# Optimization experiments

Measured on AMD Instinct MI355X. Metric: run time of the kernel, lower is better.

## Reference

```python
import jax, jax.numpy as jnp
import numpy as np

BN_EPS = 1e-5


def setup_inputs() -> dict:
    key = jax.random.key(0)
    ks = jax.random.split(key, 6)
    b, c_out, c_high = 8, 256, 512
    h1 = w1 = 64
    h2 = w2 = 32
    return {
        "fms_low": jax.random.normal(ks[0], (b, c_out, h1, w1), jnp.float32),
        "fms_high": jax.random.normal(ks[1], (b, c_high, h2, w2), jnp.float32),
        "w_conv": jax.random.normal(ks[2], (c_out, c_high), jnp.float32) * (1.0 / np.sqrt(c_high)),
        "bn_gamma": jnp.ones((c_out,), jnp.float32),
        "bn_beta": jnp.zeros((c_out,), jnp.float32),
        "bn_mean": jnp.zeros((c_out,), jnp.float32),
        "bn_var": jnp.ones((c_out,), jnp.float32),
        "fc1_w": jax.random.normal(ks[3], (c_out // 4, c_out), jnp.float32) * (1.0 / np.sqrt(c_out)),
        "fc1_b": jnp.zeros((c_out // 4,), jnp.float32),
        "fc2_w": jax.random.normal(ks[4], (c_out // 4, c_out), jnp.float32) * (1.0 / np.sqrt(c_out)),
        "fc2_b": jnp.zeros((c_out // 4,), jnp.float32),
        "scale": jax.random.normal(ks[5], (1,), jnp.float32),
    }


def reference(fms_low, fms_high, w_conv, bn_gamma, bn_beta, bn_mean, bn_var,
              fc1_w, fc1_b, fc2_w, fc2_b, scale):
    b, c, h1, w1 = fms_low.shape
    # conv_high: 1x1 conv (no bias) + BN (inference) + ReLU
    x = jnp.einsum('bchw,oc->bohw', fms_high, w_conv)  # [b, 256, h2, w2]
    inv = bn_gamma / jnp.sqrt(bn_var + BN_EPS)
    x = x * inv[None, :, None, None] + (bn_beta - bn_mean * inv)[None, :, None, None]
    x = jax.nn.relu(x)
    # raw row-major reshapes, matching torch .view(b, -1, C)
    feat_low = fms_low.reshape(b, -1, c)    # [b, N_low, 256]
    feat_high = x.reshape(b, -1, c)         # [b, N_high, 256]
    mid_low = feat_low @ fc1_w.T + fc1_b    # [b, N_low, 64]
    mid_high = feat_high @ fc2_w.T + fc2_b  # [b, N_high, 64]
    energy = jnp.einsum('bnd,bmd->bnm', mid_low, mid_high)  # [b, N_low, N_high]
    attn = jax.nn.softmax(energy, axis=-1)
    # bmm(feat_high^T, attn^T) -> [b, 256, N_low]
    mid = jnp.einsum('bmc,bnm->bcn', feat_high, attn).reshape(b, c, h1, w1)
    return scale[0] * mid
```

## Files before the change

kernel.cpp:

```cpp
#include <hip/hip_runtime.h>
#include <hip/hip_bf16.h>

typedef __bf16 v8bf __attribute__((ext_vector_type(8)));
typedef float  v4f  __attribute__((ext_vector_type(4)));

typedef __attribute__((address_space(3))) void       lds_vd;
typedef __attribute__((address_space(1))) const void gbl_vd;

#define MFMA16(a, b, c) __builtin_amdgcn_mfma_f32_16x16x32_bf16(a, b, c, 0, 0, 0)

__device__ __forceinline__ void split_hl(float v, __bf16* h, __bf16* l) {
    __bf16 hh = (__bf16)v;
    *h = hh;
    *l = (__bf16)(v - (float)hh);
}

__device__ __forceinline__ int swz_idx(int row, int col) {
    return row * 64 + ((((col >> 3) ^ (row & 7))) << 3) + (col & 7);
}
__device__ __forceinline__ const __bf16* frag_ptr(const __bf16* base, int row, int g) {
    return base + row * 64 + ((g ^ (row & 7)) << 3);
}


__global__ __launch_bounds__(256) void k_conv(
    const float* __restrict__ FH, const float* __restrict__ W,
    const float* __restrict__ gamma, const float* __restrict__ beta,
    const float* __restrict__ mean, const float* __restrict__ var,
    __bf16* __restrict__ Xhi, __bf16* __restrict__ Xlo, __bf16* __restrict__ VT)
{
    __shared__ __align__(16) __bf16 Ah[64 * 64];
    __shared__ __align__(16) __bf16 Al[64 * 64];
    __shared__ __align__(16) __bf16 Bh[64 * 64];
    __shared__ __align__(16) __bf16 Bl[64 * 64];
    __shared__ float invl[64], shl[64];

    const int tid = threadIdx.x, lane = tid & 63, w = tid >> 6;
    const int l15 = lane & 15, quad = lane >> 4;
    const int u0 = blockIdx.x * 16, o0 = blockIdx.y * 64, b = blockIdx.z;
    const float* FHb = FH + (size_t)b * 524288;

    if (tid < 64) {
        const int o = o0 + tid;
        const float iv = gamma[o] * rsqrtf(var[o] + 1e-5f);
        invl[tid] = iv;
        shl[tid] = beta[o] - mean[o] * iv;
    }

    const int ao = tid >> 2, aseg = tid & 3;
    float wreg[16], freg[16];
    {
        const float* wp = W + (size_t)(o0 + ao) * 512 + aseg * 16;
        #pragma unroll
        for (int q = 0; q < 4; ++q) {
            float4 f = ((const float4*)wp)[q];
            wreg[4*q] = f.x; wreg[4*q+1] = f.y; wreg[4*q+2] = f.z; wreg[4*q+3] = f.w;
        }
        const float* fp = FHb + (size_t)lane * 1024 + w * 256 + u0;
        #pragma unroll
        for (int q = 0; q < 4; ++q) {
            float4 f = ((const float4*)fp)[q];
            freg[4*q] = f.x; freg[4*q+1] = f.y; freg[4*q+2] = f.z; freg[4*q+3] = f.w;
        }
    }

    v4f acc[2][2];
    #pragma unroll
    for (int i = 0; i < 2; ++i)
        #pragma unroll
        for (int j = 0; j < 2; ++j) { v4f z = {0.f,0.f,0.f,0.f}; acc[i][j] = z; }
    const int oh = w >> 1, nh = w & 1;

    for (int ch = 0; ch < 8; ++ch) {
        if (ch) __syncthreads();
        #pragma unroll
        for (int z = 0; z < 2; ++z) {
            v8bf hv, lv;
            #pragma unroll
            for (int e = 0; e < 8; ++e) {
                __bf16 h, l; split_hl(wreg[8*z + e], &h, &l);
                hv[e] = h; lv[e] = l;
            }
            const int gi = (2*aseg + z) ^ (ao & 7);
            *(v8bf*)(Ah + ao*64 + (gi << 3)) = hv;
            *(v8bf*)(Al + ao*64 + (gi << 3)) = lv;
        }
        #pragma unroll
        for (int ul = 0; ul < 16; ++ul) {
            __bf16 h, l; split_hl(freg[ul], &h, &l);
            const int idx = (w*16 + ul)*64 + (((lane >> 3) ^ (ul & 7)) << 3) + (lane & 7);
            Bh[idx] = h; Bl[idx] = l;
        }
        __syncthreads();
        if (ch < 7) {
            const int c1 = (ch + 1) * 64;
            const float* wp = W + (size_t)(o0 + ao) * 512 + c1 + aseg * 16;
            #pragma unroll
            for (int q = 0; q < 4; ++q) {
                float4 f = ((const float4*)wp)[q];
                wreg[4*q] = f.x; wreg[4*q+1] = f.y; wreg[4*q+2] = f.z; wreg[4*q+3] = f.w;
            }
            const float* fp = FHb + (size_t)(c1 + lane) * 1024 + w * 256 + u0;
            #pragma unroll
            for (int q = 0; q < 4; ++q) {
                float4 f = ((const float4*)fp)[q];
                freg[4*q] = f.x; freg[4*q+1] = f.y; freg[4*q+2] = f.z; freg[4*q+3] = f.w;
            }
        }
        #pragma unroll
        for (int ks = 0; ks < 2; ++ks) {
            const int g = 4*ks + quad;
            v8bf a_h[2], a_l[2], b_h[2], b_l[2];
            #pragma unroll
            for (int i = 0; i < 2; ++i) {
                const int row = oh*32 + i*16 + l15;
                a_h[i] = *(const v8bf*)frag_ptr(Ah, row, g);
                a_l[i] = *(const v8bf*)frag_ptr(Al, row, g);
            }
            #pragma unroll
            for (int j = 0; j < 2; ++j) {
                const int row = nh*32 + j*16 + l15;
                b_h[j] = *(const v8bf*)frag_ptr(Bh, row, g);
                b_l[j] = *(const v8bf*)frag_ptr(Bl, row, g);
            }
            #pragma unroll
            for (int i = 0; i < 2; ++i)
                #pragma unroll
                for (int j = 0; j < 2; ++j) {
                    acc[i][j] = MFMA16(a_h[i], b_h[j], acc[i][j]);
                    acc[i][j] = MFMA16(a_h[i], b_l[j], acc[i][j]);
                    acc[i][j] = MFMA16(a_l[i], b_h[j], acc[i][j]);
                }
        }
    }
    __syncthreads();

    #pragma unroll
    for (int i = 0; i < 2; ++i)
        #pragma unroll
        for (int j = 0; j < 2; ++j)
            #pragma unroll
            for (int r = 0; r < 4; ++r) {
                const int row = oh*32 + i*16 + quad*4 + r;
                const int col = nh*32 + j*16 + l15;
                float v = acc[i][j][r] * invl[row] + shl[row];
                v = fmaxf(v, 0.f);
                __bf16 h, l; split_hl(v, &h, &l);
                const int idx = swz_idx(row, col);
                Ah[idx] = h; Al[idx] = l;
            }
    __syncthreads();
    {
        const int o = tid >> 2, pv = tid & 3;
        const size_t gbase = ((size_t)b*256 + o0 + o) * 1024 + pv*256 + u0;
        #pragma unroll
        for (int z = 0; z < 2; ++z) {
            const int gi = (2*pv + z) ^ (o & 7);
            v8bf h = *(v8bf*)(Ah + o*64 + (gi << 3));
            v8bf l = *(v8bf*)(Al + o*64 + (gi << 3));
            *(v8bf*)(Xhi + gbase + z*8) = h;
            *(v8bf*)(Xlo + gbase + z*8) = l;
        }
    }
    {
        const int ul = tid >> 4, s = tid & 15;
        __bf16 tmp[16];
        #pragma unroll
        for (int k = 0; k < 16; ++k) {
            const int m = s*16 + k;
            const int row = m >> 2;
            const int col = (m & 3)*16 + ul;
            tmp[k] = Ah[swz_idx(row, col)];
        }
        __bf16* vp = VT + ((size_t)b*256 + u0 + ul) * 1024 + 4*o0 + s*16;
        *(v8bf*)(vp)     = *(v8bf*)(tmp);
        *(v8bf*)(vp + 8) = *(v8bf*)(tmp + 8);
    }
}

__global__ __launch_bounds__(256) void k_proj32(
    const float* __restrict__ Feat, const float* __restrict__ Wfc,
    const float* __restrict__ bfc,
    __bf16* __restrict__ Ohi, __bf16* __restrict__ Olo)
{
    __shared__ __align__(16) __bf16 Ah[128 * 64], Al[128 * 64];
    __shared__ __align__(16) __bf16 Bh[64 * 64],  Bl[64 * 64];
    const int tid = threadIdx.x, lane = tid & 63, w = tid >> 6;
    const int l15 = lane & 15, quad = lane >> 4;
    const int r0 = blockIdx.x * 128;
    const int arow = tid >> 1, ahalf = tid & 1;
    const int brow = tid >> 2, bseg = tid & 3;

    float areg[32], breg[16];
    {
        const float* ap = Feat + (size_t)(r0 + arow) * 256 + ahalf * 32;
        #pragma unroll
        for (int q = 0; q < 8; ++q) {
            float4 f = ((const float4*)ap)[q];
            areg[4*q] = f.x; areg[4*q+1] = f.y; areg[4*q+2] = f.z; areg[4*q+3] = f.w;
        }
        const float* bp = Wfc + (size_t)brow * 256 + bseg * 16;
        #pragma unroll
        for (int q = 0; q < 4; ++q) {
            float4 f = ((const float4*)bp)[q];
            breg[4*q] = f.x; breg[4*q+1] = f.y; breg[4*q+2] = f.z; breg[4*q+3] = f.w;
        }
    }
    v4f acc[2][4];
    #pragma unroll
    for (int i = 0; i < 2; ++i)
        #pragma unroll
        for (int j = 0; j < 4; ++j) { v4f z = {0.f,0.f,0.f,0.f}; acc[i][j] = z; }

    for (int ch = 0; ch < 4; ++ch) {
        if (ch) __syncthreads();
        #pragma unroll
        for (int z = 0; z < 4; ++z) {
            v8bf hv, lv;
            #pragma unroll
            for (int e = 0; e < 8; ++e) {
                __bf16 h, l; split_hl(areg[8*z + e], &h, &l);
                hv[e] = h; lv[e] = l;
            }
            const int gi = (4*ahalf + z) ^ (arow & 7);
            *(v8bf*)(Ah + arow*64 + (gi << 3)) = hv;
            *(v8bf*)(Al + arow*64 + (gi << 3)) = lv;
        }
        #pragma unroll
        for (int z = 0; z < 2; ++z) {
            v8bf hv, lv;
            #pragma unroll
            for (int e = 0; e < 8; ++e) {
                __bf16 h, l; split_hl(breg[8*z + e], &h, &l);
                hv[e] = h; lv[e] = l;
            }
            const int gi = (2*bseg + z) ^ (brow & 7);
            *(v8bf*)(Bh + brow*64 + (gi << 3)) = hv;
            *(v8bf*)(Bl + brow*64 + (gi << 3)) = lv;
        }
        __syncthreads();
        if (ch < 3) {
            const int c1 = (ch + 1) * 64;
            const float* ap = Feat + (size_t)(r0 + arow) * 256 + c1 + ahalf * 32;
            #pragma unroll
            for (int q = 0; q < 8; ++q) {
                float4 f = ((const float4*)ap)[q];
                areg[4*q] = f.x; areg[4*q+1] = f.y; areg[4*q+2] = f.z; areg[4*q+3] = f.w;
            }
            const float* bp = Wfc + (size_t)brow * 256 + c1 + bseg * 16;
            #pragma unroll
            for (int q = 0; q < 4; ++q) {
                float4 f = ((const float4*)bp)[q];
                breg[4*q] = f.x; breg[4*q+1] = f.y; breg[4*q+2] = f.z; breg[4*q+3] = f.w;
            }
        }
        #pragma unroll
        for (int ks = 0; ks < 2; ++ks) {
            const int g = 4*ks + quad;
            v8bf a_h[2], a_l[2], b_h[4], b_l[4];
            #pragma unroll
            for (int i = 0; i < 2; ++i) {
                const int row = w*32 + i*16 + l15;
                a_h[i] = *(const v8bf*)frag_ptr(Ah, row, g);
                a_l[i] = *(const v8bf*)frag_ptr(Al, row, g);
            }
            #pragma unroll
            for (int j = 0; j < 4; ++j) {
                const int row = j*16 + l15;
                b_h[j] = *(const v8bf*)frag_ptr(Bh, row, g);
                b_l[j] = *(const v8bf*)frag_ptr(Bl, row, g);
            }
            #pragma unroll
            for (int i = 0; i < 2; ++i)
                #pragma unroll
                for (int j = 0; j < 4; ++j) {
                    acc[i][j] = MFMA16(a_h[i], b_h[j], acc[i][j]);
                    acc[i][j] = MFMA16(a_h[i], b_l[j], acc[i][j]);
                    acc[i][j] = MFMA16(a_l[i], b_h[j], acc[i][j]);
                }
        }
    }
    __syncthreads();
    #pragma unroll
    for (int j = 0; j < 4; ++j) {
        const float bias = bfc[j*16 + l15];
        #pragma unroll
        for (int i = 0; i < 2; ++i)
            #pragma unroll
            for (int r = 0; r < 4; ++r) {
                const int row = w*32 + i*16 + quad*4 + r;
                const int col = j*16 + l15;
                __bf16 h, l; split_hl(acc[i][j][r] + bias, &h, &l);
                const int idx = swz_idx(row, col);
                Ah[idx] = h; Al[idx] = l;
            }
    }
    __syncthreads();
    {
        const int row = tid >> 1, half = tid & 1;
        __bf16* oh_ = Ohi + (size_t)(r0 + row) * 64 + half * 32;
        __bf16* ol_ = Olo + (size_t)(r0 + row) * 64 + half * 32;
        #pragma unroll
        for (int z = 0; z < 4; ++z) {
            const int gi = (4*half + z) ^ (row & 7);
            *(v8bf*)(oh_ + z*8) = *(v8bf*)(Ah + row*64 + (gi << 3));
            *(v8bf*)(ol_ + z*8) = *(v8bf*)(Al + row*64 + (gi << 3));
        }
    }
}

__global__ __launch_bounds__(256) void k_projbf(
    const __bf16* __restrict__ Fhi, const __bf16* __restrict__ Flo,
    const float* __restrict__ Wfc, const float* __restrict__ bfc,
    __bf16* __restrict__ Ohi, __bf16* __restrict__ Olo)
{
    __shared__ __align__(16) __bf16 Ah[32 * 64], Al[32 * 64];
    __shared__ __align__(16) __bf16 Bh[64 * 64], Bl[64 * 64];
    const int tid = threadIdx.x, lane = tid & 63, w = tid >> 6;
    const int l15 = lane & 15, quad = lane >> 4;
    const int r0 = blockIdx.x * 32;
    const int srow = tid >> 3, sg = tid & 7;
    const int brow = tid >> 2, bseg = tid & 3;

    float breg[16];
    v8bf ha, la;
    {
        ha = *(const v8bf*)(Fhi + (size_t)(r0 + srow) * 256 + sg * 8);
        la = *(const v8bf*)(Flo + (size_t)(r0 + srow) * 256 + sg * 8);
        const float* bp = Wfc + (size_t)brow * 256 + bseg * 16;
        #pragma unroll
        for (int q = 0; q < 4; ++q) {
            float4 f = ((const float4*)bp)[q];
            breg[4*q] = f.x; breg[4*q+1] = f.y; breg[4*q+2] = f.z; breg[4*q+3] = f.w;
        }
    }
    v4f acc[2];
    { v4f z = {0.f,0.f,0.f,0.f}; acc[0] = z; acc[1] = z; }
    const int mt = w >> 1, nh = w & 1;

    for (int ch = 0; ch < 4; ++ch) {
        if (ch) __syncthreads();
        {
            const int gi = sg ^ (srow & 7);
            *(v8bf*)(Ah + srow*64 + (gi << 3)) = ha;
            *(v8bf*)(Al + srow*64 + (gi << 3)) = la;
        }
        #pragma unroll
        for (int z = 0; z < 2; ++z) {
            v8bf hv, lv;
            #pragma unroll
            for (int e = 0; e < 8; ++e) {
                __bf16 h, l; split_hl(breg[8*z + e], &h, &l);
                hv[e] = h; lv[e] = l;
            }
            const int gi = (2*bseg + z) ^ (brow & 7);
            *(v8bf*)(Bh + brow*64 + (gi << 3)) = hv;
            *(v8bf*)(Bl + brow*64 + (gi << 3)) = lv;
        }
        __syncthreads();
        if (ch < 3) {
            const int c1 = (ch + 1) * 64;
            ha = *(const v8bf*)(Fhi + (size_t)(r0 + srow) * 256 + c1 + sg * 8);
            la = *(const v8bf*)(Flo + (size_t)(r0 + srow) * 256 + c1 + sg * 8);
            const float* bp = Wfc + (size_t)brow * 256 + c1 + bseg * 16;
            #pragma unroll
            for (int q = 0; q < 4; ++q) {
                float4 f = ((const float4*)bp)[q];
                breg[4*q] = f.x; breg[4*q+1] = f.y; breg[4*q+2] = f.z; breg[4*q+3] = f.w;
            }
        }
        #pragma unroll
        for (int ks = 0; ks < 2; ++ks) {
            const int g = 4*ks + quad;
            const int arow = mt*16 + l15;
            v8bf a_h = *(const v8bf*)frag_ptr(Ah, arow, g);
            v8bf a_l = *(const v8bf*)frag_ptr(Al, arow, g);
            #pragma unroll
            for (int j = 0; j < 2; ++j) {
                const int row = (nh*2 + j)*16 + l15;
                v8bf b_h = *(const v8bf*)frag_ptr(Bh, row, g);
                v8bf b_l = *(const v8bf*)frag_ptr(Bl, row, g);
                acc[j] = MFMA16(a_h, b_h, acc[j]);
                acc[j] = MFMA16(a_h, b_l, acc[j]);
                acc[j] = MFMA16(a_l, b_h, acc[j]);
            }
        }
    }
    __syncthreads();
    #pragma unroll
    for (int j = 0; j < 2; ++j) {
        const float bias = bfc[(nh*2 + j)*16 + l15];
        #pragma unroll
        for (int r = 0; r < 4; ++r) {
            const int row = mt*16 + quad*4 + r;
            const int col = (nh*2 + j)*16 + l15;
            __bf16 h, l; split_hl(acc[j][r] + bias, &h, &l);
            const int idx = swz_idx(row, col);
            Ah[idx] = h; Al[idx] = l;
        }
    }
    __syncthreads();
    {
        const int row = tid >> 3, g = tid & 7;
        const int gi = g ^ (row & 7);
        *(v8bf*)(Ohi + (size_t)(r0 + row) * 64 + g*8) = *(v8bf*)(Ah + row*64 + (gi << 3));
        *(v8bf*)(Olo + (size_t)(r0 + row) * 64 + g*8) = *(v8bf*)(Al + row*64 + (gi << 3));
    }
}

__global__ __launch_bounds__(256, 4) void k_attn(
    const __bf16* __restrict__ MLhi, const __bf16* __restrict__ MLlo,
    const __bf16* __restrict__ MHhi, const __bf16* __restrict__ MHlo,
    const __bf16* __restrict__ VT,
    const float* __restrict__ scale_p,
    float* __restrict__ out)
{
    __shared__ __align__(16) __bf16 Khi[32 * 64];
    __shared__ __align__(16) __bf16 Klo[32 * 64];
    __shared__ __align__(16) __bf16 Vs[256 * 32];
    __shared__ __align__(16) __bf16 Ps[4][16 * 32];
    __shared__ float lsh[4][16];

    const int tid = threadIdx.x, lane = tid & 63, w = tid >> 6;
    const int l15 = lane & 15, quad = lane >> 4;
    const int b = blockIdx.x & 7, qtb = blockIdx.x >> 3;
    const int q0 = qtb * 64;

    v8bf qhi[2], qlo[2];
    {
        const __bf16* qp  = MLhi + ((size_t)(b*4096 + q0 + w*16 + l15)) * 64;
        const __bf16* qlp = MLlo + ((size_t)(b*4096 + q0 + w*16 + l15)) * 64;
        #pragma unroll
        for (int h = 0; h < 2; ++h) {
            qhi[h] = *(const v8bf*)(qp + h*32 + quad*8);
            qlo[h] = *(const v8bf*)(qlp + h*32 + quad*8);
        }
    }

    const char* Khg = (const char*)(MHhi + (size_t)b * 65536);
    const char* Klg = (const char*)(MHlo + (size_t)b * 65536);
    const char* Vg  = (const char*)(VT + (size_t)b * 262144);
    const int offK = (lane >> 3) * 128 + (((lane & 7) ^ ((lane >> 3) & 7)) << 4);
    const int offV = (lane >> 2) * 2048 + ((((lane & 3) ^ ((lane >> 3) & 3))) << 4);

    v4f oacc[4][4];
    #pragma unroll
    for (int qt = 0; qt < 4; ++qt)
        #pragma unroll
        for (int cb = 0; cb < 4; ++cb) { v4f z = {0.f,0.f,0.f,0.f}; oacc[qt][cb] = z; }
    float lrow[4] = {0.f, 0.f, 0.f, 0.f};

    for (int ch = 0; ch < 32; ++ch) {
        const int m0 = ch * 32;
        if (ch) __syncthreads();
        if (w < 4) {
            __builtin_amdgcn_global_load_lds((gbl_vd*)(Khg + m0*128 + w*1024 + offK),
                                             (lds_vd*)((char*)Khi + w*1024), 16, 0, 0);
            __builtin_amdgcn_global_load_lds((gbl_vd*)(Klg + m0*128 + w*1024 + offK),
                                             (lds_vd*)((char*)Klo + w*1024), 16, 0, 0);
        }
        #pragma unroll
        for (int i = w; i < 16; i += 4)
            __builtin_amdgcn_global_load_lds((gbl_vd*)(Vg + m0*2 + i*32768 + offV),
                                             (lds_vd*)((char*)Vs + i*1024), 16, 0, 0);
        __syncthreads();

        float S[2][4];
        #pragma unroll
        for (int mb = 0; mb < 2; ++mb) {
            v4f sacc = {0.f, 0.f, 0.f, 0.f};
            #pragma unroll
            for (int h = 0; h < 2; ++h) {
                const int row = mb*16 + l15, g = 4*h + quad;
                v8bf kh = *(const v8bf*)frag_ptr(Khi, row, g);
                v8bf kl = *(const v8bf*)frag_ptr(Klo, row, g);
                sacc = MFMA16(qhi[h], kh, sacc);
                sacc = MFMA16(qhi[h], kl, sacc);
                sacc = MFMA16(qlo[h], kh, sacc);
            }
            #pragma unroll
            for (int r = 0; r < 4; ++r) S[mb][r] = sacc[r];
        }

        #pragma unroll
        for (int mb = 0; mb < 2; ++mb)
            #pragma unroll
            for (int r = 0; r < 4; ++r) {
                const float p = __expf(S[mb][r]);
                S[mb][r] = p;
                lrow[r] += p;
            }
        #pragma unroll
        for (int mb = 0; mb < 2; ++mb)
            #pragma unroll
            for (int r = 0; r < 4; ++r) {
                const int row = quad*4 + r;
                const int slot = (mb*2 + (l15 >> 3)) ^ ((row >> 1) & 3);
                Ps[w][row*32 + (slot << 3) + (l15 & 7)] = (__bf16)S[mb][r];
            }
        __syncthreads();

        v8bf pa[4];
        #pragma unroll
        for (int qt = 0; qt < 4; ++qt)
            pa[qt] = *(const v8bf*)(Ps[qt] + l15*32 + ((quad ^ ((l15 >> 1) & 3)) << 3));
        #pragma unroll
        for (int cb = 0; cb < 4; ++cb) {
            const int vrow = w*64 + cb*16 + l15;
            v8bf vv = *(const v8bf*)(Vs + vrow*32 + ((quad ^ ((vrow >> 1) & 3)) << 3));
            #pragma unroll
            for (int qt = 0; qt < 4; ++qt)
                oacc[qt][cb] = MFMA16(pa[qt], vv, oacc[qt][cb]);
        }
    }

    #pragma unroll
    for (int r = 0; r < 4; ++r) {
        float s = lrow[r];
        #pragma unroll
        for (int d = 1; d < 16; d <<= 1) s += __shfl_xor(s, d, 64);
        lrow[r] = s;
    }
    if (l15 == 0) {
        #pragma unroll
        for (int r = 0; r < 4; ++r) lsh[w][quad*4 + r] = lrow[r];
    }
    __syncthreads();

    const float scl = scale_p[0];
    float inv[4][4];
    #pragma unroll
    for (int qt = 0; qt < 4; ++qt)
        #pragma unroll
        for (int r = 0; r < 4; ++r) inv[qt][r] = scl / lsh[qt][quad*4 + r];
    float* outb = out + (size_t)b * 256 * 4096;
    #pragma unroll
    for (int cb = 0; cb < 4; ++cb) {
        const int c = w*64 + cb*16 + l15;
        #pragma unroll
        for (int qt = 0; qt < 4; ++qt) {
            float4 v;
            v.x = oacc[qt][cb][0] * inv[qt][0];
            v.y = oacc[qt][cb][1] * inv[qt][1];
            v.z = oacc[qt][cb][2] * inv[qt][2];
            v.w = oacc[qt][cb][3] * inv[qt][3];
            *(float4*)(outb + (size_t)c * 4096 + q0 + qt*16 + quad*4) = v;
        }
    }
}

extern "C" void kernel_launch(void* const* d_in, const int* in_sizes, int n_in,
                              void* d_out, int out_size, void* d_ws, size_t ws_size,
                              hipStream_t stream)
{
    const float* fms_low  = (const float*)d_in[0];
    const float* fms_high = (const float*)d_in[1];
    const float* w_conv   = (const float*)d_in[2];
    const float* gamma    = (const float*)d_in[3];
    const float* beta     = (const float*)d_in[4];
    const float* mean     = (const float*)d_in[5];
    const float* var      = (const float*)d_in[6];
    const float* fc1_w    = (const float*)d_in[7];
    const float* fc1_b    = (const float*)d_in[8];
    const float* fc2_w    = (const float*)d_in[9];
    const float* fc2_b    = (const float*)d_in[10];
    const float* scale    = (const float*)d_in[11];
    float* out = (float*)d_out;

    __bf16* Xhi  = (__bf16*)d_ws;
    __bf16* Xlo  = Xhi  + (size_t)8*256*1024;
    __bf16* VT   = Xlo  + (size_t)8*256*1024;
    __bf16* MLhi = VT   + (size_t)8*256*1024;
    __bf16* MLlo = MLhi + (size_t)8*4096*64;
    __bf16* MHhi = MLlo + (size_t)8*4096*64;
    __bf16* MHlo = MHhi + (size_t)8*1024*64;

    k_conv<<<dim3(16, 4, 8), 256, 0, stream>>>(fms_high, w_conv, gamma, beta,
                                               mean, var, Xhi, Xlo, VT);
    k_projbf<<<dim3(256), 256, 0, stream>>>(Xhi, Xlo, fc2_w, fc2_b, MHhi, MHlo);
    k_proj32<<<dim3(256), 256, 0, stream>>>(fms_low, fc1_w, fc1_b, MLhi, MLlo);
    k_attn<<<dim3(512), 256, 0, stream>>>(MLhi, MLlo, MHhi, MHlo, VT, scale, out);
}
```

Baseline: 193.8 us.

## Double-buffer K/V tiles in attention kernel and prefetch next chunk

The attention kernel now keeps two LDS buffers for the K hi/lo and V tiles. Each iteration issues the async global-to-LDS loads for the next chunk while computing on the current one, so memory latency overlaps the MFMA work instead of stalling each iteration. It also raises wave priority around the MFMA sections and replaces the mid-loop __syncthreads with a barrier that waits only on LDS counters, so in-flight prefetches are not drained. In exchange, LDS per block roughly doubles and the launch bound drops to 2 blocks per CU, which lowers possible occupancy.

```diff
diff --git a/kernel.cpp b/kernel.cpp
--- a/kernel.cpp
+++ b/kernel.cpp
@@ -408,17 +408,17 @@
     }
 }
 
-__global__ __launch_bounds__(256, 4) void k_attn(
+__global__ __launch_bounds__(256, 2) void k_attn(
     const __bf16* __restrict__ MLhi, const __bf16* __restrict__ MLlo,
     const __bf16* __restrict__ MHhi, const __bf16* __restrict__ MHlo,
     const __bf16* __restrict__ VT,
     const float* __restrict__ scale_p,
     float* __restrict__ out)
 {
-    __shared__ __align__(16) __bf16 Khi[32 * 64];
-    __shared__ __align__(16) __bf16 Klo[32 * 64];
-    __shared__ __align__(16) __bf16 Vs[256 * 32];
-    __shared__ __align__(16) __bf16 Ps[4][16 * 32];
+    __shared__ __align__(16) __bf16 Khi[2][32 * 64];
+    __shared__ __align__(16) __bf16 Klo[2][32 * 64];
+    __shared__ __align__(16) __bf16 Vs [2][256 * 32];
+    __shared__ __align__(16) __bf16 Ps [4][16 * 32];
     __shared__ float lsh[4][16];
 
     const int tid = threadIdx.x, lane = tid & 63, w = tid >> 6;
@@ -450,30 +450,48 @@
         for (int cb = 0; cb < 4; ++cb) { v4f z = {0.f,0.f,0.f,0.f}; oacc[qt][cb] = z; }
     float lrow[4] = {0.f, 0.f, 0.f, 0.f};
 
+    {
+        __builtin_amdgcn_global_load_lds((gbl_vd*)(Khg + w*1024 + offK),
+                                         (lds_vd*)((char*)&Khi[0][0] + w*1024), 16, 0, 0);
+        __builtin_amdgcn_global_load_lds((gbl_vd*)(Klg + w*1024 + offK),
+                                         (lds_vd*)((char*)&Klo[0][0] + w*1024), 16, 0, 0);
+        #pragma unroll
+        for (int i = w; i < 16; i += 4)
+            __builtin_amdgcn_global_load_lds((gbl_vd*)(Vg + i*32768 + offV),
+                                             (lds_vd*)((char*)&Vs[0][0] + i*1024), 16, 0, 0);
+    }
+
     for (int ch = 0; ch < 32; ++ch) {
-        const int m0 = ch * 32;
-        if (ch) __syncthreads();
-        if (w < 4) {
-            __builtin_amdgcn_global_load_lds((gbl_vd*)(Khg + m0*128 + w*1024 + offK),
-                                             (lds_vd*)((char*)Khi + w*1024), 16, 0, 0);
-            __builtin_amdgcn_global_load_lds((gbl_vd*)(Klg + m0*128 + w*1024 + offK),
-                                             (lds_vd*)((char*)Klo + w*1024), 16, 0, 0);
-        }
-        #pragma unroll
-        for (int i = w; i < 16; i += 4)
-            __builtin_amdgcn_global_load_lds((gbl_vd*)(Vg + m0*2 + i*32768 + offV),
-                                             (lds_vd*)((char*)Vs + i*1024), 16, 0, 0);
+        const int cur = ch & 1;
+        const __bf16* Kh = &Khi[cur][0];
+        const __bf16* Kl = &Klo[cur][0];
+        const __bf16* Vc = &Vs[cur][0];
+
         __syncthreads();
 
+        if (ch < 31) {
+            const int m0n = (ch + 1) * 32;
+            const int nb = cur ^ 1;
+            __builtin_amdgcn_global_load_lds((gbl_vd*)(Khg + m0n*128 + w*1024 + offK),
+                                             (lds_vd*)((char*)&Khi[nb][0] + w*1024), 16, 0, 0);
+            __builtin_amdgcn_global_load_lds((gbl_vd*)(Klg + m0n*128 + w*1024 + offK),
+                                             (lds_vd*)((char*)&Klo[nb][0] + w*1024), 16, 0, 0);
+            #pragma unroll
+            for (int i = w; i < 16; i += 4)
+                __builtin_amdgcn_global_load_lds((gbl_vd*)(Vg + m0n*2 + i*32768 + offV),
+                                                 (lds_vd*)((char*)&Vs[nb][0] + i*1024), 16, 0, 0);
+        }
+
         float S[2][4];
+        __builtin_amdgcn_s_setprio(1);
         #pragma unroll
         for (int mb = 0; mb < 2; ++mb) {
             v4f sacc = {0.f, 0.f, 0.f, 0.f};
             #pragma unroll
             for (int h = 0; h < 2; ++h) {
                 const int row = mb*16 + l15, g = 4*h + quad;
-                v8bf kh = *(const v8bf*)frag_ptr(Khi, row, g);
-                v8bf kl = *(const v8bf*)frag_ptr(Klo, row, g);
+                v8bf kh = *(const v8bf*)frag_ptr(Kh, row, g);
+                v8bf kl = *(const v8bf*)frag_ptr(Kl, row, g);
                 sacc = MFMA16(qhi[h], kh, sacc);
                 sacc = MFMA16(qhi[h], kl, sacc);
                 sacc = MFMA16(qlo[h], kh, sacc);
@@ -481,6 +499,7 @@
             #pragma unroll
             for (int r = 0; r < 4; ++r) S[mb][r] = sacc[r];
         }
+        __builtin_amdgcn_s_setprio(0);
 
         #pragma unroll
         for (int mb = 0; mb < 2; ++mb)
@@ -498,20 +517,22 @@
                 const int slot = (mb*2 + (l15 >> 3)) ^ ((row >> 1) & 3);
                 Ps[w][row*32 + (slot << 3) + (l15 & 7)] = (__bf16)S[mb][r];
             }
-        __syncthreads();
+        asm volatile("s_waitcnt lgkmcnt(0)\n\ts_barrier" ::: "memory");
 
         v8bf pa[4];
         #pragma unroll
         for (int qt = 0; qt < 4; ++qt)
             pa[qt] = *(const v8bf*)(Ps[qt] + l15*32 + ((quad ^ ((l15 >> 1) & 3)) << 3));
+        __builtin_amdgcn_s_setprio(1);
         #pragma unroll
         for (int cb = 0; cb < 4; ++cb) {
             const int vrow = w*64 + cb*16 + l15;
-            v8bf vv = *(const v8bf*)(Vs + vrow*32 + ((quad ^ ((vrow >> 1) & 3)) << 3));
+            v8bf vv = *(const v8bf*)(Vc + vrow*32 + ((quad ^ ((vrow >> 1) & 3)) << 3));
             #pragma unroll
             for (int qt = 0; qt < 4; ++qt)
                 oacc[qt][cb] = MFMA16(pa[qt], vv, oacc[qt][cb]);
         }
+        __builtin_amdgcn_s_setprio(0);
     }
 
     #pragma unroll
```

Measured after the change: 186.4 us. 3.8% less time.
